# Performance work log

Measured on AMD Instinct MI355X. Metric: run time of the kernel, lower is better.

## Reference

```python
import jax, jax.numpy as jnp
import numpy as np

H = 128  # GRU units


def _gru_dir(x, W, U, b, reverse):
    """Keras GRU (reset_after=True, gate order z,r,h). x: [B,T,D].
    Returns (final_state [B,H], all_states [B,T,H])."""
    b_i, b_h = b[0], b[1]  # input bias, recurrent bias, each [3H]
    # Precompute input projections for all timesteps: [T,B,3H]
    xp = jnp.einsum('btd,dh->tbh', x, W) + b_i

    def step(h, xt):
        rec = h @ U + b_h                       # [B,3H]
        xz, xr, xh = jnp.split(xt, 3, axis=-1)
        rz, rr, rh = jnp.split(rec, 3, axis=-1)
        z = jax.nn.sigmoid(xz + rz)
        r = jax.nn.sigmoid(xr + rr)
        hh = jnp.tanh(xh + r * rh)
        hn = z * h + (1.0 - z) * hh
        return hn, hn

    h0 = jnp.zeros((x.shape[0], H), x.dtype)
    hT, hs = jax.lax.scan(step, h0, xp, reverse=reverse)
    return hT, jnp.transpose(hs, (1, 0, 2))  # [B,T,H]


def _forward(x, Ws, Us, bs, Wd, bd):
    out = x
    for l in range(3):
        fT, f = _gru_dir(out, Ws[l, 0], Us[l, 0], bs[l, 0], reverse=False)
        bT, b = _gru_dir(out, Ws[l, 1], Us[l, 1], bs[l, 1], reverse=True)
        if l < 2:  # return_sequences=True, concat merge
            out = jnp.concatenate([f, b], axis=-1)      # [B,T,2H]
        else:      # return_sequences=False: final states
            out = jnp.concatenate([fT, bT], axis=-1)    # [B,2H]
    return jax.nn.sigmoid(out @ Wd + bd)                # [B,1]


def setup_inputs() -> dict:
    key = jax.random.key(0)
    ks = jax.random.split(key, 5)
    B, T, D = 256, 512, 256
    x = jax.random.normal(ks[0], (B, T, D), jnp.float32)
    # glorot-ish scaling to keep gates in a sane range
    Ws = jax.random.normal(ks[1], (3, 2, D, 3 * H), jnp.float32) * (1.0 / np.sqrt(D))
    Us = jax.random.normal(ks[2], (3, 2, H, 3 * H), jnp.float32) * (1.0 / np.sqrt(H))
    bs = jnp.zeros((3, 2, 2, 3 * H), jnp.float32)
    Wd = jax.random.normal(ks[3], (2 * H, 1), jnp.float32) * (1.0 / np.sqrt(2 * H))
    bd = jnp.zeros((1,), jnp.float32)
    return {"x": x, "Ws": Ws, "Us": Us, "bs": bs, "Wd": Wd, "bd": bd}


def reference(x, Ws, Us, bs, Wd, bd):
    return _forward(x, Ws, Us, bs, Wd, bd)
```

## Files before the change

kernel.cpp:

```cpp
#include <hip/hip_runtime.h>
#include <hip/hip_bf16.h>

#define DEV __device__ __forceinline__

constexpr int B_ = 256;
constexpr int T_ = 512;
constexpr int H_ = 128;
constexpr int K_ = 256;
constexpr int G_ = 384;
constexpr int M_ = B_ * T_;
constexpr int LDSROW = 72;

using bf16 = __hip_bfloat16;
typedef short bf16x8 __attribute__((ext_vector_type(8)));
typedef float f32x4 __attribute__((ext_vector_type(4)));
typedef float f32x2 __attribute__((ext_vector_type(2)));

DEV float tof(float x) { return x; }
DEV float tof(bf16 x) { return __bfloat162float(x); }
DEV void stor(float* p, float v) { *p = v; }
DEV void stor(bf16* p, float v) { *p = __float2bfloat16(v); }

DEV unsigned short f2bs(float f) {
  union { float f; unsigned u; } v;
  v.f = f;
  unsigned r = (v.u + 0x7FFFu + ((v.u >> 16) & 1u)) >> 16;
  return (unsigned short)r;
}
DEV float bs2f(unsigned short s) {
  union { unsigned u; float f; } v;
  v.u = ((unsigned)s) << 16;
  return v.f;
}

DEV float fsigmoid(float x) { return 1.f / (1.f + __expf(-x)); }
DEV float ftanh(float x) {
  x = fminf(20.f, fmaxf(-20.f, x));
  float e = __expf(-2.f * x);
  return (1.f - e) / (1.f + e);
}

DEV void barrier_lds() {
  asm volatile("s_waitcnt lgkmcnt(0)\n\ts_barrier" ::: "memory");
}

DEV void pin4(float4& v) {
  asm volatile("" : "+v"(v.x), "+v"(v.y), "+v"(v.z), "+v"(v.w));
}

DEV f32x4 mfma16(bf16x8 a, bf16x8 b, f32x4 c) {
  return __builtin_amdgcn_mfma_f32_16x16x32_bf16(a, b, c, 0, 0, 0);
}

DEV float dpp_red8(float x) {
  int t;
  t = __builtin_amdgcn_update_dpp(0, __float_as_int(x), 0xB1, 0xF, 0xF, true);
  x += __int_as_float(t);
  t = __builtin_amdgcn_update_dpp(0, __float_as_int(x), 0x4E, 0xF, 0xF, true);
  x += __int_as_float(t);
  t = __builtin_amdgcn_update_dpp(0, __float_as_int(x), 0x141, 0xF, 0xF, true);
  x += __int_as_float(t);
  return x;
}

__global__ __launch_bounds__(256) void convX_kernel(
    const float* __restrict__ x, ushort* __restrict__ hiA,
    ushort* __restrict__ loA) {
  const int n4 = M_ * K_ / 4;
  for (int idx = blockIdx.x * blockDim.x + threadIdx.x; idx < n4;
       idx += gridDim.x * blockDim.x) {
    float4 v = ((const float4*)x)[idx];
    ushort4 h, l;
    h.x = f2bs(v.x); l.x = f2bs(v.x - bs2f(h.x));
    h.y = f2bs(v.y); l.y = f2bs(v.y - bs2f(h.y));
    h.z = f2bs(v.z); l.z = f2bs(v.z - bs2f(h.z));
    h.w = f2bs(v.w); l.w = f2bs(v.w - bs2f(h.w));
    ((ushort4*)hiA)[idx] = h;
    ((ushort4*)loA)[idx] = l;
  }
}

__global__ __launch_bounds__(256) void convW_kernel(
    const float* __restrict__ W, ushort* __restrict__ WhiT,
    ushort* __restrict__ WloT) {
  const int ncol = blockIdx.x;
  const int dir = ncol / G_, j = ncol % G_;
  const int k = threadIdx.x;
  const float f = W[((size_t)dir * K_ + k) * G_ + j];
  const unsigned short hi = f2bs(f);
  WhiT[(size_t)ncol * K_ + k] = hi;
  WloT[(size_t)ncol * K_ + k] = f2bs(f - bs2f(hi));
}

template <typename XT>
__global__ __launch_bounds__(256, 2) void gemm3_kernel(
    const ushort* __restrict__ Ahi, const ushort* __restrict__ Alo,
    const ushort* __restrict__ WhiT, const ushort* __restrict__ WloT,
    const float* __restrict__ bbias, XT* __restrict__ xp) {
  const int m0 = blockIdx.x * 128;
  const int n0 = blockIdx.y * 128;
  const int tid = threadIdx.x;
  const int w = tid >> 6, lane = tid & 63;
  const int wm = w >> 1, wn = w & 1;
  const int col = lane & 15, quad = lane >> 4;

  __shared__ __align__(16) ushort AH[128 * LDSROW];
  __shared__ __align__(16) ushort AL[128 * LDSROW];
  __shared__ __align__(16) ushort BH[128 * LDSROW];
  __shared__ __align__(16) ushort BL[128 * LDSROW];

  f32x4 acc[4][4];
#pragma unroll
  for (int i = 0; i < 4; ++i)
#pragma unroll
    for (int n = 0; n < 4; ++n) acc[i][n] = (f32x4){0.f, 0.f, 0.f, 0.f};

  const ushort* gsrc = (w == 0) ? Ahi : (w == 1) ? Alo : (w == 2) ? WhiT : WloT;
  ushort* lds = (w == 0) ? AH : (w == 1) ? AL : (w == 2) ? BH : BL;
  const int rbase = (w < 2) ? m0 : n0;

  for (int kb = 0; kb < K_; kb += 64) {
#pragma unroll
    for (int q = 0; q < 16; ++q) {
      const int slot = q * 64 + lane;
      const int r = slot >> 3, s = slot & 7;
      bf16x8 v = *(const bf16x8*)(gsrc + (size_t)(rbase + r) * K_ + kb + s * 8);
      *(bf16x8*)&lds[r * LDSROW + s * 8] = v;
    }
    __syncthreads();
#pragma unroll
    for (int z = 0; z < 2; ++z) {
      const int cc8 = (z * 4 + quad) * 8;
      bf16x8 ah[4], al[4], bh[4], bl[4];
#pragma unroll
      for (int i = 0; i < 4; ++i) {
        const int row = wm * 64 + i * 16 + col;
        ah[i] = *(const bf16x8*)&AH[row * LDSROW + cc8];
        al[i] = *(const bf16x8*)&AL[row * LDSROW + cc8];
      }
#pragma unroll
      for (int n = 0; n < 4; ++n) {
        const int row = wn * 64 + n * 16 + col;
        bh[n] = *(const bf16x8*)&BH[row * LDSROW + cc8];
        bl[n] = *(const bf16x8*)&BL[row * LDSROW + cc8];
      }
#pragma unroll
      for (int i = 0; i < 4; ++i)
#pragma unroll
        for (int n = 0; n < 4; ++n) {
          acc[i][n] = mfma16(ah[i], bh[n], acc[i][n]);
          acc[i][n] = mfma16(al[i], bh[n], acc[i][n]);
          acc[i][n] = mfma16(ah[i], bl[n], acc[i][n]);
        }
    }
    __syncthreads();
  }

  const int dir = (n0 >= G_) ? 1 : 0;
#pragma unroll
  for (int n = 0; n < 4; ++n) {
    const int ncol = n0 + wn * 64 + n * 16 + col;
    const int g = ncol - dir * G_;
    const float bv = bbias[dir * 2 * G_ + g];
#pragma unroll
    for (int i = 0; i < 4; ++i) {
      const int mb = m0 + wm * 64 + i * 16 + quad * 4;
#pragma unroll
      for (int r = 0; r < 4; ++r) {
        const int m = mb + r;
        const int bb = m >> 9;
        const int t = m & (T_ - 1);
        stor(xp + ((size_t)(dir * T_ + t) * B_ + bb) * G_ + g,
             acc[i][n][r] + bv);
      }
    }
  }
}

DEV float4 ldU4(const float* U, int col, int k0) {
  float4 v;
  v.x = U[(size_t)(k0 + 0) * G_ + col];
  v.y = U[(size_t)(k0 + 1) * G_ + col];
  v.z = U[(size_t)(k0 + 2) * G_ + col];
  v.w = U[(size_t)(k0 + 3) * G_ + col];
  return v;
}

template <typename XT, bool LAST>
__global__ __attribute__((amdgpu_flat_work_group_size(768, 768),
                          amdgpu_waves_per_eu(3, 3))) void rec_kernel(
    const XT* __restrict__ xp, const float* __restrict__ Ubase,
    const float* __restrict__ bbase, ushort* __restrict__ seqH,
    ushort* __restrict__ seqL, float* __restrict__ fin) {
  const int dir = blockIdx.y;
  const float* U = Ubase + dir * (H_ * G_);
  const float* bh = bbase + dir * (2 * G_) + G_;
  const int b0 = blockIdx.x * 2;
  const int tid = threadIdx.x;
  const int kc = tid & 7;
  const int cg = tid >> 3;
  const int kc4 = kc * 4;

  __shared__ __align__(16) float hbuf[2][H_];
  __shared__ float rec_s[2][G_];

#define LDU(c, i) ldU4(U, cg * 4 + (c), (i) * 32 + kc4)
  float4 u00 = LDU(0, 0), u01 = LDU(0, 1), u02 = LDU(0, 2), u03 = LDU(0, 3);
  float4 u10 = LDU(1, 0), u11 = LDU(1, 1), u12 = LDU(1, 2), u13 = LDU(1, 3);
  float4 u20 = LDU(2, 0), u21 = LDU(2, 1), u22 = LDU(2, 2), u23 = LDU(2, 3);
  float4 u30 = LDU(3, 0), u31 = LDU(3, 1), u32 = LDU(3, 2), u33 = LDU(3, 3);
#undef LDU
  pin4(u00); pin4(u01); pin4(u02); pin4(u03);
  pin4(u10); pin4(u11); pin4(u12); pin4(u13);
  pin4(u20); pin4(u21); pin4(u22); pin4(u23);
  pin4(u30); pin4(u31); pin4(u32); pin4(u33);

  const int wc = kc & 3, wr = kc >> 2;
  const float bmine = bh[cg * 4 + wc];

  const int grow = tid >> 7;
  const int gu = tid & (H_ - 1);
  const bool gateT = tid < 2 * H_;

  if (gateT) hbuf[grow][gu] = 0.f;

  const XT* xbase = xp + (size_t)(dir * T_) * B_ * G_;

  XT xzc{}, xrc{}, xhc{};
  {
    const int t0 = dir ? (T_ - 1) : 0;
    if (gateT) {
      const XT* xr_ = xbase + ((size_t)t0 * B_ + b0 + grow) * G_ + gu;
      xzc = xr_[0];
      xrc = xr_[H_];
      xhc = xr_[2 * H_];
    }
  }
  barrier_lds();

  for (int it = 0; it < T_; ++it) {
    const int t = dir ? (T_ - 1 - it) : it;

    XT xzn = xzc, xrn = xrc, xhn = xhc;
    if (gateT && (it + 1 < T_)) {
      const int tn = dir ? (t - 1) : (t + 1);
      const XT* xr_ = xbase + ((size_t)tn * B_ + b0 + grow) * G_ + gu;
      xzn = xr_[0];
      xrn = xr_[H_];
      xhn = xr_[2 * H_];
    }

    f32x2 a00 = {0.f, 0.f}, a01 = {0.f, 0.f}, a02 = {0.f, 0.f}, a03 = {0.f, 0.f};
    f32x2 a10 = {0.f, 0.f}, a11 = {0.f, 0.f}, a12 = {0.f, 0.f}, a13 = {0.f, 0.f};
#define FMA2(acc, h4, u4)                                              \
  {                                                                    \
    const f32x2* hp_ = (const f32x2*)&(h4);                            \
    const f32x2* up_ = (const f32x2*)&(u4);                            \
    acc = __builtin_elementwise_fma(hp_[0], up_[0], acc);              \
    acc = __builtin_elementwise_fma(hp_[1], up_[1], acc);              \
  }
#define DOT_I(i, uA, uB, uC, uD)                                       \
  {                                                                    \
    float4 h0 = *(const float4*)&hbuf[0][(i) * 32 + kc4];              \
    float4 h1 = *(const float4*)&hbuf[1][(i) * 32 + kc4];              \
    FMA2(a00, h0, uA) FMA2(a01, h0, uB) FMA2(a02, h0, uC)              \
    FMA2(a03, h0, uD)                                                  \
    FMA2(a10, h1, uA) FMA2(a11, h1, uB) FMA2(a12, h1, uC)              \
    FMA2(a13, h1, uD)                                                  \
  }
    DOT_I(0, u00, u10, u20, u30)
    DOT_I(1, u01, u11, u21, u31)
    DOT_I(2, u02, u12, u22, u32)
    DOT_I(3, u03, u13, u23, u33)
#undef DOT_I
#undef FMA2

    float s00 = a00.x + a00.y, s01 = a01.x + a01.y;
    float s02 = a02.x + a02.y, s03 = a03.x + a03.y;
    float s10 = a10.x + a10.y, s11 = a11.x + a11.y;
    float s12 = a12.x + a12.y, s13 = a13.x + a13.y;
    s00 = dpp_red8(s00); s01 = dpp_red8(s01);
    s02 = dpp_red8(s02); s03 = dpp_red8(s03);
    s10 = dpp_red8(s10); s11 = dpp_red8(s11);
    s12 = dpp_red8(s12); s13 = dpp_red8(s13);

    const float va = wc == 0 ? s00 : wc == 1 ? s01 : wc == 2 ? s02 : s03;
    const float vb = wc == 0 ? s10 : wc == 1 ? s11 : wc == 2 ? s12 : s13;
    rec_s[wr][cg * 4 + wc] = (wr ? vb : va) + bmine;
    barrier_lds();

    if (gateT) {
      const float xz = tof(xzc);
      const float xr = tof(xrc);
      const float xh = tof(xhc);
      const float rz = rec_s[grow][gu];
      const float rr = rec_s[grow][H_ + gu];
      const float rh = rec_s[grow][2 * H_ + gu];
      const float z = fsigmoid(xz + rz);
      const float r = fsigmoid(xr + rr);
      const float hh = ftanh(xh + r * rh);
      const float hold = hbuf[grow][gu];
      const float hn = z * hold + (1.f - z) * hh;
      hbuf[grow][gu] = hn;
      if constexpr (!LAST) {
        const size_t sidx =
            ((size_t)(b0 + grow) * T_ + t) * (2 * H_) + dir * H_ + gu;
        const unsigned short hi = f2bs(hn);
        seqH[sidx] = hi;
        seqL[sidx] = f2bs(hn - bs2f(hi));
      }
      xzc = xzn;
      xrc = xrn;
      xhc = xhn;
    }
    barrier_lds();
  }

  if constexpr (LAST) {
    if (gateT) fin[(size_t)(b0 + grow) * (2 * H_) + dir * H_ + gu] =
        hbuf[grow][gu];
  }
}

__global__ void dense_kernel(const float* __restrict__ fin,
                             const float* __restrict__ Wd,
                             const float* __restrict__ bd,
                             float* __restrict__ out) {
  __shared__ float w[2 * H_];
  const int tid = threadIdx.x;
  w[tid] = Wd[tid];
  __syncthreads();
  float s = bd[0];
  const float* row = fin + tid * (2 * H_);
#pragma unroll 8
  for (int jj = 0; jj < 2 * H_; ++jj) s = fmaf(row[jj], w[jj], s);
  out[tid] = 1.f / (1.f + __expf(-s));
}

template <typename XT>
static void run_model(const float* x, const float* Ws, const float* Us,
                      const float* bs, const float* Wd, const float* bd,
                      float* out, char* ws, hipStream_t stream) {
  const size_t xpB = (size_t)2 * T_ * B_ * G_ * sizeof(XT);
  const size_t seqB = (size_t)B_ * T_ * 2 * H_ * 2;
  XT* xp = (XT*)ws;
  ushort* sHA = (ushort*)(ws + xpB);
  ushort* sLA = (ushort*)(ws + xpB + seqB);
  ushort* sHB = (ushort*)(ws + xpB + 2 * seqB);
  ushort* sLB = (ushort*)(ws + xpB + 3 * seqB);
  ushort* WhiT = (ushort*)(ws + xpB + 4 * seqB);
  ushort* WloT = WhiT + (size_t)768 * K_;
  float* fin = (float*)(ws + xpB + 4 * seqB + (size_t)2 * 768 * K_ * 2);

  convX_kernel<<<4096, 256, 0, stream>>>(x, sHB, sLB);

  const ushort* AHs[3] = {sHB, sHA, sHB};
  const ushort* ALs[3] = {sLB, sLA, sLB};
  ushort* oH[3] = {sHA, sHB, nullptr};
  ushort* oL[3] = {sLA, sLB, nullptr};

  for (int l = 0; l < 3; ++l) {
    const float* Wl = Ws + (size_t)l * 2 * K_ * G_;
    const float* bl = bs + (size_t)l * 4 * G_;
    const float* Ul = Us + (size_t)l * 2 * H_ * G_;
    convW_kernel<<<768, 256, 0, stream>>>(Wl, WhiT, WloT);
    gemm3_kernel<XT><<<dim3(M_ / 128, 6), 256, 0, stream>>>(
        AHs[l], ALs[l], WhiT, WloT, bl, xp);
    if (l < 2)
      rec_kernel<XT, false><<<dim3(B_ / 2, 2), 768, 0, stream>>>(
          xp, Ul, bl, oH[l], oL[l], nullptr);
    else
      rec_kernel<XT, true><<<dim3(B_ / 2, 2), 768, 0, stream>>>(
          xp, Ul, bl, nullptr, nullptr, fin);
  }
  dense_kernel<<<1, B_, 0, stream>>>(fin, Wd, bd, out);
}

extern "C" void kernel_launch(void* const* d_in, const int* in_sizes, int n_in,
                              void* d_out, int out_size, void* d_ws,
                              size_t ws_size, hipStream_t stream) {
  const float* x = (const float*)d_in[0];
  const float* Ws = (const float*)d_in[1];
  const float* Us = (const float*)d_in[2];
  const float* bs = (const float*)d_in[3];
  const float* Wd = (const float*)d_in[4];
  const float* bd = (const float*)d_in[5];
  float* out = (float*)d_out;
  char* ws = (char*)d_ws;

  const size_t seqB = (size_t)B_ * T_ * 2 * H_ * 2;
  const size_t wtB = (size_t)2 * 768 * K_ * 2;
  const size_t finB = (size_t)B_ * 2 * H_ * 4;
  const size_t xp32 = (size_t)2 * T_ * B_ * G_ * 4;
  const size_t tierA = xp32 + 4 * seqB + wtB + finB;
  if (ws_size >= tierA)
    run_model<float>(x, Ws, Us, bs, Wd, bd, out, ws, stream);
  else
    run_model<bf16>(x, Ws, Us, bs, Wd, bd, out, ws, stream);
}
```

Before: 2.234 ms.

## Split recurrent weights between LDS and registers to free VGPRs

```diff
diff --git a/kernel.cpp b/kernel.cpp
--- a/kernel.cpp
+++ b/kernel.cpp
@@ -10,6 +10,7 @@
 constexpr int G_ = 384;
 constexpr int M_ = B_ * T_;
 constexpr int LDSROW = 72;
+constexpr int ULS = 76;
 
 using bf16 = __hip_bfloat16;
 typedef short bf16x8 __attribute__((ext_vector_type(8)));
@@ -42,10 +43,6 @@
 
 DEV void barrier_lds() {
   asm volatile("s_waitcnt lgkmcnt(0)\n\ts_barrier" ::: "memory");
-}
-
-DEV void pin4(float4& v) {
-  asm volatile("" : "+v"(v.x), "+v"(v.y), "+v"(v.z), "+v"(v.w));
 }
 
 DEV f32x4 mfma16(bf16x8 a, bf16x8 b, f32x4 c) {
@@ -92,6 +89,15 @@
   WloT[(size_t)ncol * K_ + k] = f2bs(f - bs2f(hi));
 }
 
+__global__ __launch_bounds__(128) void convU_kernel(
+    const float* __restrict__ U, float* __restrict__ UT) {
+  const int col = blockIdx.x;
+  const int dir = blockIdx.y;
+  const int k = threadIdx.x;
+  UT[((size_t)dir * G_ + col) * H_ + k] =
+      U[(size_t)dir * H_ * G_ + (size_t)k * G_ + col];
+}
+
 template <typename XT>
 __global__ __launch_bounds__(256, 2) void gemm3_kernel(
     const ushort* __restrict__ Ahi, const ushort* __restrict__ Alo,
@@ -177,46 +183,49 @@
   }
 }
 
-DEV float4 ldU4(const float* U, int col, int k0) {
-  float4 v;
-  v.x = U[(size_t)(k0 + 0) * G_ + col];
-  v.y = U[(size_t)(k0 + 1) * G_ + col];
-  v.z = U[(size_t)(k0 + 2) * G_ + col];
-  v.w = U[(size_t)(k0 + 3) * G_ + col];
-  return v;
-}
-
 template <typename XT, bool LAST>
-__global__ __attribute__((amdgpu_flat_work_group_size(768, 768),
-                          amdgpu_waves_per_eu(3, 3))) void rec_kernel(
-    const XT* __restrict__ xp, const float* __restrict__ Ubase,
+__global__ __launch_bounds__(768, 3) void rec_kernel(
+    const XT* __restrict__ xp, const float* UTbase,
     const float* __restrict__ bbase, ushort* __restrict__ seqH,
     ushort* __restrict__ seqL, float* __restrict__ fin) {
   const int dir = blockIdx.y;
-  const float* U = Ubase + dir * (H_ * G_);
+  const float* UT = UTbase + (size_t)dir * G_ * H_;
   const float* bh = bbase + dir * (2 * G_) + G_;
   const int b0 = blockIdx.x * 2;
   const int tid = threadIdx.x;
   const int kc = tid & 7;
   const int cg = tid >> 3;
   const int kc4 = kc * 4;
+  const int c0 = cg * 4;
 
   __shared__ __align__(16) float hbuf[2][H_];
   __shared__ float rec_s[2][G_];
-
-#define LDU(c, i) ldU4(U, cg * 4 + (c), (i) * 32 + kc4)
-  float4 u00 = LDU(0, 0), u01 = LDU(0, 1), u02 = LDU(0, 2), u03 = LDU(0, 3);
-  float4 u10 = LDU(1, 0), u11 = LDU(1, 1), u12 = LDU(1, 2), u13 = LDU(1, 3);
-  float4 u20 = LDU(2, 0), u21 = LDU(2, 1), u22 = LDU(2, 2), u23 = LDU(2, 3);
-  float4 u30 = LDU(3, 0), u31 = LDU(3, 1), u32 = LDU(3, 2), u33 = LDU(3, 3);
-#undef LDU
-  pin4(u00); pin4(u01); pin4(u02); pin4(u03);
-  pin4(u10); pin4(u11); pin4(u12); pin4(u13);
-  pin4(u20); pin4(u21); pin4(u22); pin4(u23);
-  pin4(u30); pin4(u31); pin4(u32); pin4(u33);
+  __shared__ __align__(16) float Ulds[G_ * ULS];
+
+#pragma unroll
+  for (int q = 0; q < 8; ++q) {
+    const int id = q * 768 + tid;
+    const int row = id >> 4, c16 = id & 15;
+    *(float4*)&Ulds[row * ULS + c16 * 4] =
+        *(const float4*)&UT[(size_t)row * H_ + c16 * 4];
+  }
+
+  f32x2 r0a, r0b, r1a, r1b, r2a, r2b, r3a, r3b;
+  f32x2 s0a, s0b, s1a, s1b, s2a, s2b, s3a, s3b;
+#define LDR(c, base, ra, rb)                                         \
+  {                                                                  \
+    float4 t_ = *(const float4*)&UT[(size_t)(c0 + (c)) * H_ + (base) + kc4]; \
+    ra = (f32x2){t_.x, t_.y};                                        \
+    rb = (f32x2){t_.z, t_.w};                                        \
+  }
+  LDR(0, 64, r0a, r0b) LDR(1, 64, r1a, r1b)
+  LDR(2, 64, r2a, r2b) LDR(3, 64, r3a, r3b)
+  LDR(0, 96, s0a, s0b) LDR(1, 96, s1a, s1b)
+  LDR(2, 96, s2a, s2b) LDR(3, 96, s3a, s3b)
+#undef LDR
 
   const int wc = kc & 3, wr = kc >> 2;
-  const float bmine = bh[cg * 4 + wc];
+  const float bmine = bh[c0 + wc];
 
   const int grow = tid >> 7;
   const int gu = tid & (H_ - 1);
@@ -252,28 +261,82 @@
 
     f32x2 a00 = {0.f, 0.f}, a01 = {0.f, 0.f}, a02 = {0.f, 0.f}, a03 = {0.f, 0.f};
     f32x2 a10 = {0.f, 0.f}, a11 = {0.f, 0.f}, a12 = {0.f, 0.f}, a13 = {0.f, 0.f};
-#define FMA2(acc, h4, u4)                                              \
-  {                                                                    \
-    const f32x2* hp_ = (const f32x2*)&(h4);                            \
-    const f32x2* up_ = (const f32x2*)&(u4);                            \
-    acc = __builtin_elementwise_fma(hp_[0], up_[0], acc);              \
-    acc = __builtin_elementwise_fma(hp_[1], up_[1], acc);              \
-  }
-#define DOT_I(i, uA, uB, uC, uD)                                       \
-  {                                                                    \
-    float4 h0 = *(const float4*)&hbuf[0][(i) * 32 + kc4];              \
-    float4 h1 = *(const float4*)&hbuf[1][(i) * 32 + kc4];              \
-    FMA2(a00, h0, uA) FMA2(a01, h0, uB) FMA2(a02, h0, uC)              \
-    FMA2(a03, h0, uD)                                                  \
-    FMA2(a10, h1, uA) FMA2(a11, h1, uB) FMA2(a12, h1, uC)              \
-    FMA2(a13, h1, uD)                                                  \
-  }
-    DOT_I(0, u00, u10, u20, u30)
-    DOT_I(1, u01, u11, u21, u31)
-    DOT_I(2, u02, u12, u22, u32)
-    DOT_I(3, u03, u13, u23, u33)
-#undef DOT_I
-#undef FMA2
+
+#pragma unroll
+    for (int i = 0; i < 2; ++i) {
+      float4 h0 = *(const float4*)&hbuf[0][i * 32 + kc4];
+      float4 h1 = *(const float4*)&hbuf[1][i * 32 + kc4];
+      f32x2 h0a = {h0.x, h0.y}, h0b = {h0.z, h0.w};
+      f32x2 h1a = {h1.x, h1.y}, h1b = {h1.z, h1.w};
+      float4 u0 = *(const float4*)&Ulds[(c0 + 0) * ULS + i * 32 + kc4];
+      float4 u1 = *(const float4*)&Ulds[(c0 + 1) * ULS + i * 32 + kc4];
+      float4 u2 = *(const float4*)&Ulds[(c0 + 2) * ULS + i * 32 + kc4];
+      float4 u3 = *(const float4*)&Ulds[(c0 + 3) * ULS + i * 32 + kc4];
+      f32x2 u0a = {u0.x, u0.y}, u0b = {u0.z, u0.w};
+      f32x2 u1a = {u1.x, u1.y}, u1b = {u1.z, u1.w};
+      f32x2 u2a = {u2.x, u2.y}, u2b = {u2.z, u2.w};
+      f32x2 u3a = {u3.x, u3.y}, u3b = {u3.z, u3.w};
+      a00 = __builtin_elementwise_fma(h0a, u0a, a00);
+      a00 = __builtin_elementwise_fma(h0b, u0b, a00);
+      a01 = __builtin_elementwise_fma(h0a, u1a, a01);
+      a01 = __builtin_elementwise_fma(h0b, u1b, a01);
+      a02 = __builtin_elementwise_fma(h0a, u2a, a02);
+      a02 = __builtin_elementwise_fma(h0b, u2b, a02);
+      a03 = __builtin_elementwise_fma(h0a, u3a, a03);
+      a03 = __builtin_elementwise_fma(h0b, u3b, a03);
+      a10 = __builtin_elementwise_fma(h1a, u0a, a10);
+      a10 = __builtin_elementwise_fma(h1b, u0b, a10);
+      a11 = __builtin_elementwise_fma(h1a, u1a, a11);
+      a11 = __builtin_elementwise_fma(h1b, u1b, a11);
+      a12 = __builtin_elementwise_fma(h1a, u2a, a12);
+      a12 = __builtin_elementwise_fma(h1b, u2b, a12);
+      a13 = __builtin_elementwise_fma(h1a, u3a, a13);
+      a13 = __builtin_elementwise_fma(h1b, u3b, a13);
+    }
+    {
+      float4 h0 = *(const float4*)&hbuf[0][64 + kc4];
+      float4 h1 = *(const float4*)&hbuf[1][64 + kc4];
+      f32x2 h0a = {h0.x, h0.y}, h0b = {h0.z, h0.w};
+      f32x2 h1a = {h1.x, h1.y}, h1b = {h1.z, h1.w};
+      a00 = __builtin_elementwise_fma(h0a, r0a, a00);
+      a00 = __builtin_elementwise_fma(h0b, r0b, a00);
+      a01 = __builtin_elementwise_fma(h0a, r1a, a01);
+      a01 = __builtin_elementwise_fma(h0b, r1b, a01);
+      a02 = __builtin_elementwise_fma(h0a, r2a, a02);
+      a02 = __builtin_elementwise_fma(h0b, r2b, a02);
+      a03 = __builtin_elementwise_fma(h0a, r3a, a03);
+      a03 = __builtin_elementwise_fma(h0b, r3b, a03);
+      a10 = __builtin_elementwise_fma(h1a, r0a, a10);
+      a10 = __builtin_elementwise_fma(h1b, r0b, a10);
+      a11 = __builtin_elementwise_fma(h1a, r1a, a11);
+      a11 = __builtin_elementwise_fma(h1b, r1b, a11);
+      a12 = __builtin_elementwise_fma(h1a, r2a, a12);
+      a12 = __builtin_elementwise_fma(h1b, r2b, a12);
+      a13 = __builtin_elementwise_fma(h1a, r3a, a13);
+      a13 = __builtin_elementwise_fma(h1b, r3b, a13);
+    }
+    {
+      float4 h0 = *(const float4*)&hbuf[0][96 + kc4];
+      float4 h1 = *(const float4*)&hbuf[1][96 + kc4];
+      f32x2 h0a = {h0.x, h0.y}, h0b = {h0.z, h0.w};
+      f32x2 h1a = {h1.x, h1.y}, h1b = {h1.z, h1.w};
+      a00 = __builtin_elementwise_fma(h0a, s0a, a00);
+      a00 = __builtin_elementwise_fma(h0b, s0b, a00);
+      a01 = __builtin_elementwise_fma(h0a, s1a, a01);
+      a01 = __builtin_elementwise_fma(h0b, s1b, a01);
+      a02 = __builtin_elementwise_fma(h0a, s2a, a02);
+      a02 = __builtin_elementwise_fma(h0b, s2b, a02);
+      a03 = __builtin_elementwise_fma(h0a, s3a, a03);
+      a03 = __builtin_elementwise_fma(h0b, s3b, a03);
+      a10 = __builtin_elementwise_fma(h1a, s0a, a10);
+      a10 = __builtin_elementwise_fma(h1b, s0b, a10);
+      a11 = __builtin_elementwise_fma(h1a, s1a, a11);
+      a11 = __builtin_elementwise_fma(h1b, s1b, a11);
+      a12 = __builtin_elementwise_fma(h1a, s2a, a12);
+      a12 = __builtin_elementwise_fma(h1b, s2b, a12);
+      a13 = __builtin_elementwise_fma(h1a, s3a, a13);
+      a13 = __builtin_elementwise_fma(h1b, s3b, a13);
+    }
 
     float s00 = a00.x + a00.y, s01 = a01.x + a01.y;
     float s02 = a02.x + a02.y, s03 = a03.x + a03.y;
@@ -286,7 +349,7 @@
 
     const float va = wc == 0 ? s00 : wc == 1 ? s01 : wc == 2 ? s02 : s03;
     const float vb = wc == 0 ? s10 : wc == 1 ? s11 : wc == 2 ? s12 : s13;
-    rec_s[wr][cg * 4 + wc] = (wr ? vb : va) + bmine;
+    rec_s[wr][c0 + wc] = (wr ? vb : va) + bmine;
     barrier_lds();
 
     if (gateT) {
@@ -343,6 +406,7 @@
                       float* out, char* ws, hipStream_t stream) {
   const size_t xpB = (size_t)2 * T_ * B_ * G_ * sizeof(XT);
   const size_t seqB = (size_t)B_ * T_ * 2 * H_ * 2;
+  const size_t wtB = (size_t)2 * 768 * K_ * 2;
   XT* xp = (XT*)ws;
   ushort* sHA = (ushort*)(ws + xpB);
   ushort* sLA = (ushort*)(ws + xpB + seqB);
@@ -350,7 +414,8 @@
   ushort* sLB = (ushort*)(ws + xpB + 3 * seqB);
   ushort* WhiT = (ushort*)(ws + xpB + 4 * seqB);
   ushort* WloT = WhiT + (size_t)768 * K_;
-  float* fin = (float*)(ws + xpB + 4 * seqB + (size_t)2 * 768 * K_ * 2);
+  float* UT = (float*)(ws + xpB + 4 * seqB + wtB);
+  float* fin = (float*)(ws + xpB + 4 * seqB + wtB + (size_t)2 * G_ * H_ * 4);
 
   convX_kernel<<<4096, 256, 0, stream>>>(x, sHB, sLB);
 
@@ -364,14 +429,15 @@
     const float* bl = bs + (size_t)l * 4 * G_;
     const float* Ul = Us + (size_t)l * 2 * H_ * G_;
     convW_kernel<<<768, 256, 0, stream>>>(Wl, WhiT, WloT);
+    convU_kernel<<<dim3(G_, 2), 128, 0, stream>>>(Ul, UT);
     gemm3_kernel<XT><<<dim3(M_ / 128, 6), 256, 0, stream>>>(
         AHs[l], ALs[l], WhiT, WloT, bl, xp);
     if (l < 2)
       rec_kernel<XT, false><<<dim3(B_ / 2, 2), 768, 0, stream>>>(
-          xp, Ul, bl, oH[l], oL[l], nullptr);
+          xp, UT, bl, oH[l], oL[l], nullptr);
     else
       rec_kernel<XT, true><<<dim3(B_ / 2, 2), 768, 0, stream>>>(
-          xp, Ul, bl, nullptr, nullptr, fin);
+          xp, UT, bl, nullptr, nullptr, fin);
   }
   dense_kernel<<<1, B_, 0, stream>>>(fin, Wd, bd, out);
 }
@@ -390,9 +456,10 @@
 
   const size_t seqB = (size_t)B_ * T_ * 2 * H_ * 2;
   const size_t wtB = (size_t)2 * 768 * K_ * 2;
+  const size_t utB = (size_t)2 * G_ * H_ * 4;
   const size_t finB = (size_t)B_ * 2 * H_ * 4;
   const size_t xp32 = (size_t)2 * T_ * B_ * G_ * 4;
-  const size_t tierA = xp32 + 4 * seqB + wtB + finB;
+  const size_t tierA = xp32 + 4 * seqB + wtB + utB + finB;
   if (ws_size >= tierA)
     run_model<float>(x, Ws, Us, bs, Wd, bd, out, ws, stream);
   else
```

New measurement: 2.645 ms. +18.4%, slower.
